# Kernel tuning notes

Measured on AMD Instinct MI355X. Metric: run time of the kernel, lower is better.

## Reference

```python
import jax, jax.numpy as jnp
import numpy as np

N_EDGES = 100000
N_TRIP = 1000000
N_QUAD = 2000000
E, QIN, QOUT = 512, 32, 32
RBF, CBF, SBF, NSPH = 16, 16, 32, 7
KMAX, KAVG = 32, 20
INV_SQRT2 = 1.0 / np.sqrt(2.0)


def setup_inputs() -> dict:
    key = jax.random.key(0)
    ks = jax.random.split(key, 16)

    def w(k, i, o):
        return jax.random.normal(k, (i, o), jnp.float32) / np.sqrt(i).astype(np.float32)

    return {
        "m": jax.random.normal(ks[0], (N_EDGES, E), jnp.float32),
        "rad": jax.random.normal(ks[1], (N_EDGES, RBF), jnp.float32),
        "cir": jax.random.normal(ks[2], (N_TRIP, CBF), jnp.float32),
        "sph_rad_W1": jax.random.normal(ks[3], (N_EDGES, SBF, NSPH), jnp.float32),
        "sph": jax.random.normal(ks[4], (N_EDGES, KMAX, NSPH), jnp.float32),
        "W_db": w(ks[5], E, E),
        "W_rbf": w(ks[6], RBF, E),
        "W_down": w(ks[7], E, QIN),
        "W_cbf": w(ks[8], CBF, QIN),
        "W_bil": w(ks[9], SBF * QIN, QOUT),
        "W_up_ca": w(ks[10], QOUT, E),
        "W_up_ac": w(ks[11], QOUT, E),
        "scale_rbf": jnp.ones((1,), jnp.float32),
        "scale_cbf": jnp.ones((1,), jnp.float32),
        "scale_sbf": jnp.ones((1,), jnp.float32),
        "idx_trip_in": jax.random.randint(ks[12], (N_TRIP,), 0, N_EDGES, jnp.int32),
        "idx_trip_to_quad": jax.random.randint(ks[13], (N_QUAD,), 0, N_TRIP, jnp.int32),
        # ragged layout: each edge owns KAVG quadruplet slots (unique pairs, no collisions)
        "idx_out": (jnp.arange(N_QUAD, dtype=jnp.int32) // KAVG),
        "idx_out_agg": (jnp.arange(N_QUAD, dtype=jnp.int32) % KAVG),
        "id_swap": jax.random.permutation(ks[14], N_EDGES).astype(jnp.int32),
    }


def reference(m, rad, cir, sph_rad_W1, sph, W_db, W_rbf, W_down, W_cbf, W_bil,
              W_up_ca, W_up_ac, scale_rbf, scale_cbf, scale_sbf,
              idx_trip_in, idx_trip_to_quad, idx_out, idx_out_agg, id_swap):
    silu = jax.nn.silu
    x_db = silu(m @ W_db)                                # dense_db          (nE, E)
    x_db = (x_db * (rad @ W_rbf)) * scale_rbf            # mlp_rbf + scale_rbf
    x_db = silu(x_db @ W_down)                           # down_projection   (nE, QIN)
    x_db = x_db[idx_trip_in]                             # gather edge->trip (nTrip, QIN)
    x_db = (x_db * (cir @ W_cbf)) * scale_cbf            # mlp_cbf + scale_cbf
    x_db = x_db[idx_trip_to_quad]                        # gather trip->quad (nQuad, QIN)
    # EfficientInteractionBilinear: ragged scatter into (nE, Kmax, QIN), contract bases
    nE, Kmax, _ = sph.shape
    m_pad = jnp.zeros((nE, Kmax, x_db.shape[-1]), x_db.dtype)
    m_pad = m_pad.at[idx_out, idx_out_agg].set(x_db)
    sum_k = jnp.einsum('eks,ekd->esd', sph, m_pad)       # (nE, NSPH, QIN)
    rW = jnp.einsum('eis,esd->eid', sph_rad_W1, sum_k)   # (nE, SBF, QIN)
    x = (rW.reshape(nE, -1) @ W_bil) * scale_sbf         # bilinear + scale_sbf_sum (nE, QOUT)
    x_ca = silu(x @ W_up_ca)                             # up_projection_ca
    x_ac = silu(x @ W_up_ac)[id_swap]                    # up_projection_ac + swap
    return (x_ca + x_ac) * INV_SQRT2
```

## Files before the change

### kernel.cpp

```cpp
#include <hip/hip_runtime.h>
#include <hip/hip_bf16.h>


constexpr int NE   = 100000;
constexpr int NEP  = 100096;
constexpr int ED   = 512;
constexpr int NT   = 1000000;
constexpr int NQ   = 2000000;
constexpr int QI   = 32;
constexpr int QO   = 32;
constexpr int RBF_ = 16;
constexpr int CBF_ = 16;
constexpr int SBF_ = 32;
constexpr int NSPH_= 7;
constexpr int KAVG_= 20;

typedef float f32x4 __attribute__((ext_vector_type(4)));
typedef __bf16 bf16x8 __attribute__((ext_vector_type(8)));
typedef __bf16 bf16x4 __attribute__((ext_vector_type(4)));

__device__ __forceinline__ float silu_f(float v) {
    return __fdividef(v, 1.0f + __expf(-v));
}

__device__ __forceinline__ void gload_lds16(const __bf16* g, __bf16* l) {
    __builtin_amdgcn_global_load_lds(
        (const __attribute__((address_space(1))) void*)g,
        (__attribute__((address_space(3))) void*)l, 16, 0, 0);
}

__global__ __launch_bounds__(256) void k0(const float* __restrict__ mM,
                                          const float* __restrict__ Wdb,
                                          const float* __restrict__ rad,
                                          const float* __restrict__ Wrbf,
                                          __bf16* __restrict__ mB,
                                          __bf16* __restrict__ WdbT,
                                          __bf16* __restrict__ radp,
                                          __bf16* __restrict__ WrbfT)
{
    const int b = blockIdx.x, tid = threadIdx.x;
    if (b < 1600) {
        const long total = (long)NEP * ED / 8;
        for (long g = (long)b * 256 + tid; g < total; g += 409600L) {
            const long e0 = g * 8;
            const int row = (int)(e0 >> 9);
            bf16x8 o;
            if (row < NE) {
                const float4 v0 = *(const float4*)(mM + e0);
                const float4 v1 = *(const float4*)(mM + e0 + 4);
                o[0] = (__bf16)v0.x; o[1] = (__bf16)v0.y;
                o[2] = (__bf16)v0.z; o[3] = (__bf16)v0.w;
                o[4] = (__bf16)v1.x; o[5] = (__bf16)v1.y;
                o[6] = (__bf16)v1.z; o[7] = (__bf16)v1.w;
            } else {
#pragma unroll
                for (int j = 0; j < 8; j++) o[j] = (__bf16)0.f;
            }
            *(bf16x8*)(mB + e0) = o;
        }
    } else if (b < 1664) {
        __shared__ float tle[64 * 65];
        const int idx = b - 1600;
        const int kb = (idx >> 3) * 64, nb = (idx & 7) * 64;
#pragma unroll
        for (int f = tid; f < 1024; f += 256) {
            const int kk = f >> 4, n4 = (f & 15) * 4;
            const float4 v = *(const float4*)(Wdb + (size_t)(kb + kk) * ED + nb + n4);
            tle[(n4 + 0) * 65 + kk] = v.x;
            tle[(n4 + 1) * 65 + kk] = v.y;
            tle[(n4 + 2) * 65 + kk] = v.z;
            tle[(n4 + 3) * 65 + kk] = v.w;
        }
        __syncthreads();
#pragma unroll
        for (int f = tid; f < 1024; f += 256) {
            const int nn = f >> 4, k4 = (f & 15) * 4;
            bf16x4 o;
            o[0] = (__bf16)tle[nn * 65 + k4 + 0];
            o[1] = (__bf16)tle[nn * 65 + k4 + 1];
            o[2] = (__bf16)tle[nn * 65 + k4 + 2];
            o[3] = (__bf16)tle[nn * 65 + k4 + 3];
            *(bf16x4*)(WdbT + (size_t)(nb + nn) * ED + kb + k4) = o;
        }
    } else if (b < 2064) {
        for (int g = (b - 1664) * 256 + tid; g < NEP * 8; g += 102400) {
            const int row = g >> 3, c = g & 7;
            bf16x8 o;
            if (row < NE && c < 2) {
                const float* s = rad + (size_t)row * RBF_ + c * 8;
                const float4 v0 = *(const float4*)s;
                const float4 v1 = *(const float4*)(s + 4);
                o[0] = (__bf16)v0.x; o[1] = (__bf16)v0.y;
                o[2] = (__bf16)v0.z; o[3] = (__bf16)v0.w;
                o[4] = (__bf16)v1.x; o[5] = (__bf16)v1.y;
                o[6] = (__bf16)v1.z; o[7] = (__bf16)v1.w;
            } else {
#pragma unroll
                for (int j = 0; j < 8; j++) o[j] = (__bf16)0.f;
            }
            *(bf16x8*)(radp + (size_t)row * 64 + c * 8) = o;
        }
    } else {
        for (int f = (b - 2064) * 256 + tid; f < 512 * 64; f += 4096) {
            const int n = f >> 6, k = f & 63;
            const float v = (k < RBF_) ? Wrbf[(size_t)k * ED + n] : 0.f;
            WrbfT[(size_t)n * 64 + k] = (__bf16)v;
        }
    }
}

__global__ __launch_bounds__(256) void k1(const __bf16* __restrict__ mB,
                                          const __bf16* __restrict__ WdbT,
                                          const __bf16* __restrict__ radp,
                                          const __bf16* __restrict__ WrbfT,
                                          const float* __restrict__ s_rbf,
                                          __bf16* __restrict__ x1)
{
    __shared__ __align__(16) __bf16 As[128 * 64];
    __shared__ __align__(16) __bf16 Bs[128 * 64];

    const int tid  = threadIdx.x;
    const int lane = tid & 63, wv = tid >> 6;
    const int ml = lane & 15, qd = lane >> 4;
    const int col0 = blockIdx.x * 128;
    const int row0 = blockIdx.y * 128;
    const int wm = (wv >> 1) * 64, wn = (wv & 1) * 64;

    const int sr  = lane >> 3;
    const int scs = (lane & 7) ^ sr;
    const int swr = ml & 7;

    f32x4 acc[4][4], accR[4][4];
    const f32x4 vz = {0.f, 0.f, 0.f, 0.f};
#pragma unroll
    for (int i = 0; i < 4; i++)
#pragma unroll
        for (int j = 0; j < 4; j++) { acc[i][j] = vz; accR[i][j] = vz; }

    const __bf16* aT = mB    + (size_t)row0 * ED;
    const __bf16* bT = WdbT  + (size_t)col0 * ED;
    const __bf16* aR = radp  + (size_t)row0 * 64;
    const __bf16* bR = WrbfT + (size_t)col0 * 64;

    for (int k0 = 0; k0 < ED; k0 += 64) {
        __syncthreads();
#pragma unroll
        for (int j = 0; j < 4; j++) {
            const int i = wv * 4 + j;
            const int r = i * 8 + sr;
            gload_lds16(aT + (size_t)r * ED + k0 + scs * 8, &As[i * 512]);
            gload_lds16(bT + (size_t)r * ED + k0 + scs * 8, &Bs[i * 512]);
        }
        __syncthreads();
#pragma unroll
        for (int kk = 0; kk < 2; kk++) {
            const int co = (((kk << 2) + qd) ^ swr) << 3;
            bf16x8 af[4], bg[4];
#pragma unroll
            for (int t = 0; t < 4; t++) {
                af[t] = *(const bf16x8*)&As[(wm + t * 16 + ml) * 64 + co];
                bg[t] = *(const bf16x8*)&Bs[(wn + t * 16 + ml) * 64 + co];
            }
#pragma unroll
            for (int mt = 0; mt < 4; mt++)
#pragma unroll
                for (int nt = 0; nt < 4; nt++)
                    acc[mt][nt] = __builtin_amdgcn_mfma_f32_16x16x32_bf16(
                        af[mt], bg[nt], acc[mt][nt], 0, 0, 0);
        }
    }

    __syncthreads();
#pragma unroll
    for (int j = 0; j < 4; j++) {
        const int i = wv * 4 + j;
        const int r = i * 8 + sr;
        gload_lds16(aR + (size_t)r * 64 + scs * 8, &As[i * 512]);
        gload_lds16(bR + (size_t)r * 64 + scs * 8, &Bs[i * 512]);
    }
    __syncthreads();
    {
        const int co = (qd ^ swr) << 3;
        bf16x8 af[4], bg[4];
#pragma unroll
        for (int t = 0; t < 4; t++) {
            af[t] = *(const bf16x8*)&As[(wm + t * 16 + ml) * 64 + co];
            bg[t] = *(const bf16x8*)&Bs[(wn + t * 16 + ml) * 64 + co];
        }
#pragma unroll
        for (int mt = 0; mt < 4; mt++)
#pragma unroll
            for (int nt = 0; nt < 4; nt++)
                accR[mt][nt] = __builtin_amdgcn_mfma_f32_16x16x32_bf16(
                    af[mt], bg[nt], accR[mt][nt], 0, 0, 0);
    }

    const float srbf = s_rbf[0];
#pragma unroll
    for (int mt = 0; mt < 4; mt++)
#pragma unroll
        for (int r = 0; r < 4; r++) {
            const int grow = row0 + wm + mt * 16 + qd * 4 + r;
            if (grow < NE) {
#pragma unroll
                for (int nt = 0; nt < 4; nt++) {
                    const int cc = col0 + wn + nt * 16 + ml;
                    float v = silu_f(acc[mt][nt][r]) * accR[mt][nt][r] * srbf;
                    x1[(size_t)grow * ED + cc] = (__bf16)v;
                }
            }
        }
}

__global__ __launch_bounds__(256) void k2(const __bf16* __restrict__ x1,
                                          const float* __restrict__ Wdown,
                                          __bf16* __restrict__ x2)
{
    constexpr int BM = 128, BK = 64, LPA = 72, LPB = 72;
    __shared__ __bf16 As[BM * LPA];
    __shared__ __bf16 Bs[QI * LPB];

    const int tid = threadIdx.x;
    const int lane = tid & 63, wv = tid >> 6;
    const int ml = lane & 15, qd = lane >> 4;
    const int row0 = blockIdx.x * BM;
    const int wm = wv * 32;

    f32x4 acc[2][2];
    const f32x4 vz = {0.f, 0.f, 0.f, 0.f};
#pragma unroll
    for (int i = 0; i < 2; i++) { acc[i][0] = vz; acc[i][1] = vz; }

    for (int k0 = 0; k0 < ED; k0 += BK) {
        __syncthreads();
#pragma unroll
        for (int f = tid; f < 1024; f += 256) {
            int r = f >> 3, c8 = (f & 7) * 8;
            uint4 v = make_uint4(0u, 0u, 0u, 0u);
            if (row0 + r < NE) v = *(const uint4*)(x1 + (size_t)(row0 + r) * ED + k0 + c8);
            *(uint4*)&As[r * LPA + c8] = v;
        }
#pragma unroll
        for (int f = tid; f < BK * QI; f += 256) {
            int kr = f >> 5, c = f & 31;
            Bs[c * LPB + kr] = (__bf16)Wdown[(size_t)(k0 + kr) * QI + c];
        }
        __syncthreads();
#pragma unroll
        for (int kk = 0; kk < 2; kk++) {
            bf16x8 b0 = *(const bf16x8*)&Bs[(0  + ml) * LPB + kk * 32 + qd * 8];
            bf16x8 b1 = *(const bf16x8*)&Bs[(16 + ml) * LPB + kk * 32 + qd * 8];
#pragma unroll
            for (int mt = 0; mt < 2; mt++) {
                bf16x8 a = *(const bf16x8*)&As[(wm + mt * 16 + ml) * LPA + kk * 32 + qd * 8];
                acc[mt][0] = __builtin_amdgcn_mfma_f32_16x16x32_bf16(a, b0, acc[mt][0], 0, 0, 0);
                acc[mt][1] = __builtin_amdgcn_mfma_f32_16x16x32_bf16(a, b1, acc[mt][1], 0, 0, 0);
            }
        }
    }
#pragma unroll
    for (int mt = 0; mt < 2; mt++)
#pragma unroll
        for (int nt = 0; nt < 2; nt++)
#pragma unroll
            for (int r = 0; r < 4; r++) {
                int grow = row0 + wm + mt * 16 + qd * 4 + r;
                int cc = nt * 16 + ml;
                if (grow < NE) x2[(size_t)grow * QI + cc] = (__bf16)silu_f(acc[mt][nt][r]);
            }
}

__global__ __launch_bounds__(256) void k3(const float* __restrict__ cir,
                                          const float* __restrict__ Wcbf,
                                          const float* __restrict__ s_cbf,
                                          const int* __restrict__ trip_in,
                                          const __bf16* __restrict__ x2,
                                          __bf16* __restrict__ t)
{
    constexpr int TPB = 64;
    __shared__ float cirs[TPB * CBF_];
    __shared__ float wc[CBF_ * QI];
    __shared__ int eix[TPB];

    const int tid = threadIdx.x;
    const int t0 = blockIdx.x * TPB;
#pragma unroll
    for (int i = tid; i < TPB * CBF_; i += 256) {
        int r = i >> 4, c = i & 15;
        cirs[i] = cir[(size_t)(t0 + r) * CBF_ + c];
    }
#pragma unroll
    for (int i = tid; i < CBF_ * QI; i += 256) wc[i] = Wcbf[i];
    if (tid < TPB) eix[tid] = trip_in[t0 + tid];
    __syncthreads();

    const float sc = s_cbf[0];
    const int d = tid & 31, ts0 = tid >> 5;
#pragma unroll
    for (int p = 0; p < TPB / 8; p++) {
        int ts = ts0 + p * 8;
        float a = 0.f;
#pragma unroll
        for (int c = 0; c < CBF_; c++) a += cirs[ts * CBF_ + c] * wc[c * QI + d];
        float xv = (float)x2[(size_t)eix[ts] * QI + d];
        t[(size_t)(t0 + ts) * QI + d] = (__bf16)(xv * a * sc);
    }
}

__global__ __launch_bounds__(256) void k4(const __bf16* __restrict__ t,
                                          const float* __restrict__ sph,
                                          const float* __restrict__ sphW1,
                                          const float* __restrict__ Wbil,
                                          const float* __restrict__ s_sbf,
                                          const int* __restrict__ t2q,
                                          float* __restrict__ x)
{
    constexpr int BE = 32;
    __shared__ float sumk[BE * NSPH_ * 32];
    __shared__ float sphs[BE * KAVG_ * NSPH_];
    __shared__ int   qidx[BE * KAVG_];
    __shared__ __bf16 rws[32 * 72];
    __shared__ __bf16 wbs[32 * 72];

    const int tid = threadIdx.x;
    const int e0 = blockIdx.x * BE;
    const int d = tid & 31, eg = tid >> 5;
    const int lane = tid & 63, wv = tid >> 6;
    const int ml = lane & 15, qd = lane >> 4;
    const int mt = wv & 1, nt = wv >> 1;

    for (int i = tid; i < BE * KAVG_ * NSPH_; i += 256) {
        int e = i / (KAVG_ * NSPH_), rem = i % (KAVG_ * NSPH_);
        sphs[i] = sph[((size_t)(e0 + e) * 32) * NSPH_ + rem];
    }
    for (int i = tid; i < BE * KAVG_; i += 256) qidx[i] = t2q[(size_t)e0 * KAVG_ + i];
    __syncthreads();

    for (int e = eg; e < BE; e += 8) {
        float a[NSPH_] = {0.f, 0.f, 0.f, 0.f, 0.f, 0.f, 0.f};
        for (int k = 0; k < KAVG_; k++) {
            int q = qidx[e * KAVG_ + k];
            float tv = (float)t[(size_t)q * QI + d];
            const float* s7 = &sphs[(e * KAVG_ + k) * NSPH_];
#pragma unroll
            for (int s = 0; s < NSPH_; s++) a[s] += s7[s] * tv;
        }
#pragma unroll
        for (int s = 0; s < NSPH_; s++) sumk[(e * NSPH_ + s) * 32 + d] = a[s];
    }
    __syncthreads();

    f32x4 acc = {0.f, 0.f, 0.f, 0.f};
    for (int kc = 0; kc < 16; kc++) {
        __syncthreads();
#pragma unroll
        for (int j = 0; j < 4; j++) {
            int e = eg + 8 * j;
#pragma unroll
            for (int is = 0; is < 2; is++) {
                int i = kc * 2 + is;
                const float* w1 = &sphW1[((size_t)(e0 + e) * SBF_ + i) * NSPH_];
                float v = 0.f;
#pragma unroll
                for (int s = 0; s < NSPH_; s++) v += w1[s] * sumk[(e * NSPH_ + s) * 32 + d];
                rws[e * 72 + is * 32 + d] = (__bf16)v;
            }
        }
#pragma unroll
        for (int f = tid; f < 2048; f += 256) {
            int kr = f >> 5, o = f & 31;
            wbs[o * 72 + kr] = (__bf16)Wbil[(size_t)(kc * 64 + kr) * QO + o];
        }
        __syncthreads();
#pragma unroll
        for (int kk = 0; kk < 2; kk++) {
            bf16x8 a = *(const bf16x8*)&rws[(mt * 16 + ml) * 72 + kk * 32 + qd * 8];
            bf16x8 b = *(const bf16x8*)&wbs[(nt * 16 + ml) * 72 + kk * 32 + qd * 8];
            acc = __builtin_amdgcn_mfma_f32_16x16x32_bf16(a, b, acc, 0, 0, 0);
        }
    }
    const float ssb = s_sbf[0];
#pragma unroll
    for (int r = 0; r < 4; r++) {
        int e = mt * 16 + qd * 4 + r, o = nt * 16 + ml;
        x[(size_t)(e0 + e) * QO + o] = acc[r] * ssb;
    }
}

__global__ __launch_bounds__(256) void k5(const float* __restrict__ x,
                                          const float* __restrict__ Wca,
                                          const float* __restrict__ Wac,
                                          const int* __restrict__ swp,
                                          float* __restrict__ outp)
{
    constexpr int BM = 128, BN = 128, LP = 40;
    __shared__ __bf16 Aca[BM * LP];
    __shared__ __bf16 Aac[BM * LP];
    __shared__ __bf16 Bca[BN * LP];
    __shared__ __bf16 Bac[BN * LP];

    const int tid = threadIdx.x;
    const int lane = tid & 63, wv = tid >> 6;
    const int ml = lane & 15, qd = lane >> 4;
    const int row0 = blockIdx.x * BM, col0 = blockIdx.y * BN;
    const int wm = (wv >> 1) * 64, wn = (wv & 1) * 64;

#pragma unroll
    for (int f = tid; f < BM * 8; f += 256) {
        int r = f >> 3, c4 = (f & 7) * 4;
        int grow = row0 + r;
        float4 v = make_float4(0.f, 0.f, 0.f, 0.f);
        float4 w = make_float4(0.f, 0.f, 0.f, 0.f);
        if (grow < NE) {
            v = *(const float4*)(x + (size_t)grow * QI + c4);
            int sr = swp[grow];
            w = *(const float4*)(x + (size_t)sr * QI + c4);
        }
        __bf16* dv = &Aca[r * LP + c4];
        dv[0] = (__bf16)v.x; dv[1] = (__bf16)v.y; dv[2] = (__bf16)v.z; dv[3] = (__bf16)v.w;
        __bf16* dw = &Aac[r * LP + c4];
        dw[0] = (__bf16)w.x; dw[1] = (__bf16)w.y; dw[2] = (__bf16)w.z; dw[3] = (__bf16)w.w;
    }
#pragma unroll
    for (int f = tid; f < 1024; f += 256) {
        int kr = f >> 5, c4 = (f & 31) * 4;
        float4 v = *(const float4*)(Wca + (size_t)kr * ED + col0 + c4);
        float4 w = *(const float4*)(Wac + (size_t)kr * ED + col0 + c4);
        Bca[(c4 + 0) * LP + kr] = (__bf16)v.x;
        Bca[(c4 + 1) * LP + kr] = (__bf16)v.y;
        Bca[(c4 + 2) * LP + kr] = (__bf16)v.z;
        Bca[(c4 + 3) * LP + kr] = (__bf16)v.w;
        Bac[(c4 + 0) * LP + kr] = (__bf16)w.x;
        Bac[(c4 + 1) * LP + kr] = (__bf16)w.y;
        Bac[(c4 + 2) * LP + kr] = (__bf16)w.z;
        Bac[(c4 + 3) * LP + kr] = (__bf16)w.w;
    }
    __syncthreads();

    f32x4 aC[4][4], aA[4][4];
    const f32x4 vz = {0.f, 0.f, 0.f, 0.f};
#pragma unroll
    for (int i = 0; i < 4; i++)
#pragma unroll
        for (int j = 0; j < 4; j++) { aC[i][j] = vz; aA[i][j] = vz; }

    bf16x8 afC[4], afA[4], bfC[4], bfA[4];
#pragma unroll
    for (int i = 0; i < 4; i++) {
        afC[i] = *(const bf16x8*)&Aca[(wm + i * 16 + ml) * LP + qd * 8];
        afA[i] = *(const bf16x8*)&Aac[(wm + i * 16 + ml) * LP + qd * 8];
        bfC[i] = *(const bf16x8*)&Bca[(wn + i * 16 + ml) * LP + qd * 8];
        bfA[i] = *(const bf16x8*)&Bac[(wn + i * 16 + ml) * LP + qd * 8];
    }
#pragma unroll
    for (int mt = 0; mt < 4; mt++)
#pragma unroll
        for (int nt = 0; nt < 4; nt++) {
            aC[mt][nt] = __builtin_amdgcn_mfma_f32_16x16x32_bf16(afC[mt], bfC[nt], aC[mt][nt], 0, 0, 0);
            aA[mt][nt] = __builtin_amdgcn_mfma_f32_16x16x32_bf16(afA[mt], bfA[nt], aA[mt][nt], 0, 0, 0);
        }

    const float inv_sqrt2 = 0.70710678118654752440f;
#pragma unroll
    for (int mt = 0; mt < 4; mt++)
#pragma unroll
        for (int r = 0; r < 4; r++) {
            int grow = row0 + wm + mt * 16 + qd * 4 + r;
            if (grow < NE) {
#pragma unroll
                for (int nt = 0; nt < 4; nt++) {
                    int cc = wn + nt * 16 + ml;
                    float v = (silu_f(aC[mt][nt][r]) + silu_f(aA[mt][nt][r])) * inv_sqrt2;
                    outp[(size_t)grow * ED + col0 + cc] = v;
                }
            }
        }
}

extern "C" void kernel_launch(void* const* d_in, const int* in_sizes, int n_in,
                              void* d_out, int out_size, void* d_ws, size_t ws_size,
                              hipStream_t stream)
{
    (void)in_sizes; (void)n_in; (void)out_size; (void)ws_size;

    const float* mM    = (const float*)d_in[0];
    const float* rad   = (const float*)d_in[1];
    const float* cir   = (const float*)d_in[2];
    const float* sphW1 = (const float*)d_in[3];
    const float* sph   = (const float*)d_in[4];
    const float* Wdb   = (const float*)d_in[5];
    const float* Wrbf  = (const float*)d_in[6];
    const float* Wdown = (const float*)d_in[7];
    const float* Wcbf  = (const float*)d_in[8];
    const float* Wbil  = (const float*)d_in[9];
    const float* Wca   = (const float*)d_in[10];
    const float* Wac   = (const float*)d_in[11];
    const float* s_rbf = (const float*)d_in[12];
    const float* s_cbf = (const float*)d_in[13];
    const float* s_sbf = (const float*)d_in[14];
    const int* trip_in = (const int*)d_in[15];
    const int* t2q     = (const int*)d_in[16];
    const int* swp     = (const int*)d_in[19];

    char* ws = (char*)d_ws;
    __bf16* x1 = (__bf16*)(ws);
    __bf16* x2 = (__bf16*)(ws + 102400000);
    __bf16* tt = (__bf16*)(ws + 108800000);
    float*  xx = (float*) (ws + 172800000);

    __bf16* mB    = (__bf16*)d_out;
    __bf16* WdbT  = (__bf16*)(ws + 108800000);
    __bf16* radp  = (__bf16*)(ws + 108800000 + 524288);
    __bf16* WrbfT = (__bf16*)(ws + 108800000 + 524288 + 12812288);

    constexpr int GM = (NE + 127) / 128;

    k0<<<2080, 256, 0, stream>>>(mM, Wdb, rad, Wrbf, mB, WdbT, radp, WrbfT);
    k1<<<dim3(4, GM), 256, 0, stream>>>(mB, WdbT, radp, WrbfT, s_rbf, x1);
    k2<<<GM, 256, 0, stream>>>(x1, Wdown, x2);
    k3<<<NT / 64, 256, 0, stream>>>(cir, Wcbf, s_cbf, trip_in, x2, tt);
    k4<<<NE / 32, 256, 0, stream>>>(tt, sph, sphW1, Wbil, s_sbf, t2q, xx);
    k5<<<dim3(GM, 4), 256, 0, stream>>>(xx, Wca, Wac, swp, (float*)d_out);
}
```

Baseline: 1.048 ms.

## Split bilinear kernel into gather-sum and contraction kernels with pre-transposed W_bil

The fused k4 kernel is split in two. k4a gathers quadruplet rows with 4-wide bf16 vector loads, one 8-thread group per edge, and writes sum_k to global memory. k4b loads sum_k and sph_rad_W1 tiles into LDS with float4 loads, keeps sum_k in registers, and reads a W_bil that k0 now pre-transposes to bf16, replacing the strided fp32 transpose that ran every k-chunk. This is meant to raise parallelism and coalescing in the gather phase and cut redundant weight conversion, at the cost of an extra kernel launch and a round trip of sum_k through global memory.

```diff
diff --git a/kernel.cpp b/kernel.cpp
--- a/kernel.cpp
+++ b/kernel.cpp
@@ -33,10 +33,12 @@
                                           const float* __restrict__ Wdb,
                                           const float* __restrict__ rad,
                                           const float* __restrict__ Wrbf,
+                                          const float* __restrict__ Wbil,
                                           __bf16* __restrict__ mB,
                                           __bf16* __restrict__ WdbT,
                                           __bf16* __restrict__ radp,
-                                          __bf16* __restrict__ WrbfT)
+                                          __bf16* __restrict__ WrbfT,
+                                          __bf16* __restrict__ WbilT)
 {
     const int b = blockIdx.x, tid = threadIdx.x;
     if (b < 1600) {
@@ -100,11 +102,16 @@
             }
             *(bf16x8*)(radp + (size_t)row * 64 + c * 8) = o;
         }
-    } else {
+    } else if (b < 2080) {
         for (int f = (b - 2064) * 256 + tid; f < 512 * 64; f += 4096) {
             const int n = f >> 6, k = f & 63;
             const float v = (k < RBF_) ? Wrbf[(size_t)k * ED + n] : 0.f;
             WrbfT[(size_t)n * 64 + k] = (__bf16)v;
+        }
+    } else {
+        for (int f = (b - 2080) * 256 + tid; f < 32 * 1024; f += 2048) {
+            const int o = f >> 10, k = f & 1023;
+            WbilT[(size_t)o * 1024 + k] = (__bf16)Wbil[(size_t)k * QO + o];
         }
     }
 }
@@ -307,70 +314,103 @@
     }
 }
 
-__global__ __launch_bounds__(256) void k4(const __bf16* __restrict__ t,
-                                          const float* __restrict__ sph,
-                                          const float* __restrict__ sphW1,
-                                          const float* __restrict__ Wbil,
-                                          const float* __restrict__ s_sbf,
-                                          const int* __restrict__ t2q,
-                                          float* __restrict__ x)
-{
-    constexpr int BE = 32;
-    __shared__ float sumk[BE * NSPH_ * 32];
-    __shared__ float sphs[BE * KAVG_ * NSPH_];
-    __shared__ int   qidx[BE * KAVG_];
+__global__ __launch_bounds__(256, 4) void k4a(const __bf16* __restrict__ t,
+                                              const float* __restrict__ sph,
+                                              const int* __restrict__ t2q,
+                                              float* __restrict__ sumk)
+{
+    __shared__ float sphs[32 * KAVG_ * NSPH_];
+    __shared__ int   qidx[32 * KAVG_];
+
+    const int tid = threadIdx.x;
+    const int e0 = blockIdx.x * 32;
+
+    for (int i = tid; i < 32 * KAVG_ * NSPH_; i += 256) {
+        int e = i / (KAVG_ * NSPH_), rem = i % (KAVG_ * NSPH_);
+        sphs[i] = sph[((size_t)(e0 + e) * 32) * NSPH_ + rem];
+    }
+    for (int i = tid; i < 32 * KAVG_; i += 256) qidx[i] = t2q[(size_t)e0 * KAVG_ + i];
+    __syncthreads();
+
+    const int g = tid >> 3;
+    const int dq = (tid & 7) * 4;
+
+    f32x4 a[NSPH_];
+#pragma unroll
+    for (int s = 0; s < NSPH_; s++) a[s] = (f32x4){0.f, 0.f, 0.f, 0.f};
+
+#pragma unroll
+    for (int k = 0; k < KAVG_; k++) {
+        const int q = qidx[g * KAVG_ + k];
+        const bf16x4 tv = *(const bf16x4*)(t + (size_t)q * QI + dq);
+        f32x4 tf;
+#pragma unroll
+        for (int j = 0; j < 4; j++) tf[j] = (float)tv[j];
+        const float* s7 = &sphs[(g * KAVG_ + k) * NSPH_];
+#pragma unroll
+        for (int s = 0; s < NSPH_; s++) {
+            const float w = s7[s];
+#pragma unroll
+            for (int j = 0; j < 4; j++) a[s][j] += w * tf[j];
+        }
+    }
+#pragma unroll
+    for (int s = 0; s < NSPH_; s++)
+        *(f32x4*)(sumk + ((size_t)(e0 + g) * NSPH_ + s) * 32 + dq) = a[s];
+}
+
+__global__ __launch_bounds__(256) void k4b(const float* __restrict__ sumk,
+                                           const float* __restrict__ sphW1,
+                                           const __bf16* __restrict__ WbilT,
+                                           const float* __restrict__ s_sbf,
+                                           float* __restrict__ x)
+{
+    __shared__ float sks[32 * NSPH_ * 32];
+    __shared__ float w1s[32 * SBF_ * NSPH_];
     __shared__ __bf16 rws[32 * 72];
     __shared__ __bf16 wbs[32 * 72];
 
     const int tid = threadIdx.x;
-    const int e0 = blockIdx.x * BE;
+    const int e0 = blockIdx.x * 32;
+
+    for (int i = tid; i < 1792; i += 256) {
+        *(float4*)&sks[i * 4] = *(const float4*)(sumk  + (size_t)e0 * 224 + i * 4);
+        *(float4*)&w1s[i * 4] = *(const float4*)(sphW1 + (size_t)e0 * 224 + i * 4);
+    }
+    __syncthreads();
+
     const int d = tid & 31, eg = tid >> 5;
     const int lane = tid & 63, wv = tid >> 6;
     const int ml = lane & 15, qd = lane >> 4;
     const int mt = wv & 1, nt = wv >> 1;
 
-    for (int i = tid; i < BE * KAVG_ * NSPH_; i += 256) {
-        int e = i / (KAVG_ * NSPH_), rem = i % (KAVG_ * NSPH_);
-        sphs[i] = sph[((size_t)(e0 + e) * 32) * NSPH_ + rem];
-    }
-    for (int i = tid; i < BE * KAVG_; i += 256) qidx[i] = t2q[(size_t)e0 * KAVG_ + i];
-    __syncthreads();
-
-    for (int e = eg; e < BE; e += 8) {
-        float a[NSPH_] = {0.f, 0.f, 0.f, 0.f, 0.f, 0.f, 0.f};
-        for (int k = 0; k < KAVG_; k++) {
-            int q = qidx[e * KAVG_ + k];
-            float tv = (float)t[(size_t)q * QI + d];
-            const float* s7 = &sphs[(e * KAVG_ + k) * NSPH_];
-#pragma unroll
-            for (int s = 0; s < NSPH_; s++) a[s] += s7[s] * tv;
-        }
-#pragma unroll
-        for (int s = 0; s < NSPH_; s++) sumk[(e * NSPH_ + s) * 32 + d] = a[s];
-    }
-    __syncthreads();
+    float sk[4][NSPH_];
+#pragma unroll
+    for (int j = 0; j < 4; j++)
+#pragma unroll
+        for (int s = 0; s < NSPH_; s++)
+            sk[j][s] = sks[((eg + 8 * j) * NSPH_ + s) * 32 + d];
+
+    const int wo = tid >> 3, wc8 = (tid & 7) * 8;
 
     f32x4 acc = {0.f, 0.f, 0.f, 0.f};
     for (int kc = 0; kc < 16; kc++) {
         __syncthreads();
 #pragma unroll
         for (int j = 0; j < 4; j++) {
-            int e = eg + 8 * j;
+            const int e = eg + 8 * j;
 #pragma unroll
             for (int is = 0; is < 2; is++) {
-                int i = kc * 2 + is;
-                const float* w1 = &sphW1[((size_t)(e0 + e) * SBF_ + i) * NSPH_];
+                const int i = kc * 2 + is;
+                const float* w1 = &w1s[(e * SBF_ + i) * NSPH_];
                 float v = 0.f;
 #pragma unroll
-                for (int s = 0; s < NSPH_; s++) v += w1[s] * sumk[(e * NSPH_ + s) * 32 + d];
+                for (int s = 0; s < NSPH_; s++) v += w1[s] * sk[j][s];
                 rws[e * 72 + is * 32 + d] = (__bf16)v;
             }
         }
-#pragma unroll
-        for (int f = tid; f < 2048; f += 256) {
-            int kr = f >> 5, o = f & 31;
-            wbs[o * 72 + kr] = (__bf16)Wbil[(size_t)(kc * 64 + kr) * QO + o];
-        }
+        *(bf16x8*)&wbs[wo * 72 + wc8] =
+            *(const bf16x8*)(WbilT + (size_t)wo * 1024 + kc * 64 + wc8);
         __syncthreads();
 #pragma unroll
         for (int kk = 0; kk < 2; kk++) {
@@ -507,18 +547,21 @@
     __bf16* x2 = (__bf16*)(ws + 102400000);
     __bf16* tt = (__bf16*)(ws + 108800000);
     float*  xx = (float*) (ws + 172800000);
+    float*  smk= (float*) (ws);
 
     __bf16* mB    = (__bf16*)d_out;
+    __bf16* WbilT = (__bf16*)((char*)d_out + 103000000);
     __bf16* WdbT  = (__bf16*)(ws + 108800000);
     __bf16* radp  = (__bf16*)(ws + 108800000 + 524288);
     __bf16* WrbfT = (__bf16*)(ws + 108800000 + 524288 + 12812288);
 
     constexpr int GM = (NE + 127) / 128;
 
-    k0<<<2080, 256, 0, stream>>>(mM, Wdb, rad, Wrbf, mB, WdbT, radp, WrbfT);
+    k0<<<2088, 256, 0, stream>>>(mM, Wdb, rad, Wrbf, Wbil, mB, WdbT, radp, WrbfT, WbilT);
     k1<<<dim3(4, GM), 256, 0, stream>>>(mB, WdbT, radp, WrbfT, s_rbf, x1);
     k2<<<GM, 256, 0, stream>>>(x1, Wdown, x2);
     k3<<<NT / 64, 256, 0, stream>>>(cir, Wcbf, s_cbf, trip_in, x2, tt);
-    k4<<<NE / 32, 256, 0, stream>>>(tt, sph, sphW1, Wbil, s_sbf, t2q, xx);
+    k4a<<<NE / 32, 256, 0, stream>>>(tt, sph, t2q, smk);
+    k4b<<<NE / 32, 256, 0, stream>>>(smk, sphW1, WbilT, s_sbf, xx);
     k5<<<dim3(GM, 4), 256, 0, stream>>>(xx, Wca, Wac, swp, (float*)d_out);
 }
```

Result: faster. 941.4 us (-10.2%).
